# Optimization experiments

Hardware: AMD Instinct MI355X
Metric: run time of the kernel (lower is better)

The kernel has to match this reference:

```python
import jax, jax.numpy as jnp
import numpy as np
from jax import lax

WIN = 9  # box-filter window per spatial dim
PAD = WIN // 2


def _box_sum(x, filt):
    # x: [N,1,D,H,W]; uniform ones filter -> local sums, 'same' padding
    return lax.conv_general_dilated(
        x, filt, window_strides=(1, 1, 1),
        padding=[(PAD, PAD)] * 3,
        dimension_numbers=("NCDHW", "OIDHW", "NCDHW"))


def l_ncc(I, J):
    filt = jnp.ones((1, 1, WIN, WIN, WIN), dtype=I.dtype)
    win_size = float(WIN ** 3)
    I_sum = _box_sum(I, filt)
    J_sum = _box_sum(J, filt)
    I2_sum = _box_sum(I * I, filt)
    J2_sum = _box_sum(J * J, filt)
    IJ_sum = _box_sum(I * J, filt)
    u_I = I_sum / win_size
    u_J = J_sum / win_size
    cross = IJ_sum - u_J * I_sum - u_I * J_sum + u_I * u_J * win_size
    I_var = I2_sum - 2.0 * u_I * I_sum + u_I * u_I * win_size
    J_var = J2_sum - 2.0 * u_J * J_sum + u_J * u_J * win_size
    cc = cross * cross / (I_var * J_var + 1e-5)
    return 1.0 - jnp.mean(cc)


def l_mse(y_true, y_pred):
    return jnp.mean((y_true - y_pred) ** 2)


def l_smooth(s):
    # squared forward differences along the three spatial axes of [N,C,D,H,W]
    dy = s[..., 1:, :, :] - s[..., :-1, :, :]
    dx = s[..., :, 1:, :] - s[..., :, :-1, :]
    dz = s[..., :, :, 1:] - s[..., :, :, :-1]
    d = jnp.mean(dx * dx) + jnp.mean(dy * dy) + jnp.mean(dz * dz)
    return d / 3.0


def setup_inputs() -> dict:
    key = jax.random.key(0)
    k1, k2, k3, k4 = jax.random.split(key, 4)
    shp = (2, 1, 128, 128, 128)
    return {
        "imgsA": jax.random.uniform(k1, shp, dtype=jnp.float32),
        "recon_A": jax.random.uniform(k2, shp, dtype=jnp.float32),
        "warped_BA": jax.random.uniform(k3, shp, dtype=jnp.float32),
        "flow_BA": jax.random.normal(k4, (2, 3, 128, 128, 128), dtype=jnp.float32),
    }


def reference(imgsA, recon_A, warped_BA, flow_BA):
    ncc_loss = l_ncc(warped_BA, imgsA)
    mse_loss = l_mse(imgsA, recon_A)
    smooth_loss = l_smooth(flow_BA)
    return (ncc_loss, mse_loss, smooth_loss)
```

## Files before the change

### kernel.cpp

```cpp
#include <hip/hip_runtime.h>

#define VOL   4194304
#define FLOWN 12582912
#define SMCNT 12484608.0f
#define WIN_INV (1.0f / 729.0f)

__device__ __forceinline__ void block_reduce_atomic(float v, float* red, float* dst) {
#pragma unroll
    for (int off = 32; off; off >>= 1) v += __shfl_down(v, off);
    if ((threadIdx.x & 63) == 0) red[threadIdx.x >> 6] = v;
    __syncthreads();
    if (threadIdx.x == 0) atomicAdd(dst, red[0] + red[1] + red[2] + red[3]);
}

struct __align__(16) NccLds {
    float wst[2][5][16][25];
    float hst[2][5][16][16];
};

#define WSLIDE(c, X0,X1,X2,X3,X4,X5,X6,X7,X8,X9,X10,X11)                   \
    {                                                                      \
        const float o0 = X0+X1+X2+X3+X4+X5+X6+X7+X8;                       \
        const float o1 = o0 - X0 + X9;                                     \
        const float o2 = o1 - X1 + X10;                                    \
        const float o3 = o2 - X2 + X11;                                    \
        L->wst[wpl][c][wq4 + 0][wrr] = o0;                                 \
        L->wst[wpl][c][wq4 + 1][wrr] = o1;                                 \
        L->wst[wpl][c][wq4 + 2][wrr] = o2;                                 \
        L->wst[wpl][c][wq4 + 3][wrr] = o3;                                 \
    }

#define EMIT {                                                             \
        const float cross = S[4] - S[0] * S[1] * WIN_INV;                  \
        const float iv    = S[2] - S[0] * S[0] * WIN_INV;                  \
        const float jv    = S[3] - S[1] * S[1] * WIN_INV;                  \
        local += cross * cross / (iv * jv + 1e-5f);                       \
    }

#define NCC_PAIR(PP, R0, R1, R2, R3, R4, R5)                                   \
    {                                                                          \
        const int pp = (PP);                                                   \
        {                                                                      \
            const int dp = d0 - 4 + 2 * pp + wpl;                              \
            if (tid < 192 && (unsigned)dp < 128u) {                            \
                const float4 i0 = R0, i1 = R1, i2 = R2;                        \
                const float4 j0 = R3, j1 = R4, j2 = R5;                        \
                WSLIDE(0, i0.x,i0.y,i0.z,i0.w, i1.x,i1.y,i1.z,i1.w,            \
                          i2.x,i2.y,i2.z,i2.w)                                 \
                WSLIDE(1, j0.x,j0.y,j0.z,j0.w, j1.x,j1.y,j1.z,j1.w,            \
                          j2.x,j2.y,j2.z,j2.w)                                 \
                WSLIDE(2, i0.x*i0.x,i0.y*i0.y,i0.z*i0.z,i0.w*i0.w,             \
                          i1.x*i1.x,i1.y*i1.y,i1.z*i1.z,i1.w*i1.w,             \
                          i2.x*i2.x,i2.y*i2.y,i2.z*i2.z,i2.w*i2.w)             \
                WSLIDE(3, j0.x*j0.x,j0.y*j0.y,j0.z*j0.z,j0.w*j0.w,             \
                          j1.x*j1.x,j1.y*j1.y,j1.z*j1.z,j1.w*j1.w,             \
                          j2.x*j2.x,j2.y*j2.y,j2.z*j2.z,j2.w*j2.w)             \
                WSLIDE(4, i0.x*j0.x,i0.y*j0.y,i0.z*j0.z,i0.w*j0.w,             \
                          i1.x*j1.x,i1.y*j1.y,i1.z*j1.z,i1.w*j1.w,             \
                          i2.x*j2.x,i2.y*j2.y,i2.z*j2.z,i2.w*j2.w)             \
            }                                                                  \
        }                                                                      \
        if (pp + 2 < 36) issue6(pp + 2, R0, R1, R2, R3, R4, R5);               \
        __syncthreads();                                                       \
        _Pragma("unroll")                                                      \
        for (int rep = 0; rep < 3; ++rep) {                                    \
            int id = -1;                                                       \
            if (rep < 2) id = tid + rep * 256;                                 \
            else if (tid >= 128) id = 384 + tid;                               \
            if (id >= 0 && id < 640) {                                         \
                const int pl = id >= 320;                                      \
                const int r2 = id - pl * 320;                                  \
                const int c  = r2 >> 6;                                        \
                const int w  = (r2 >> 2) & 15;                                 \
                const int qh = r2 & 3;                                         \
                const int dp = d0 - 4 + 2 * pp + pl;                           \
                if ((unsigned)dp < 128u) {                                     \
                    const float* sp = &L->wst[pl][c][w][qh << 2];              \
                    const float4 a0 = *(const float4*)sp;                      \
                    const float4 a1 = *(const float4*)(sp + 4);                \
                    const float4 a2 = *(const float4*)(sp + 8);                \
                    const float o0 = a0.x+a0.y+a0.z+a0.w+a1.x+a1.y+a1.z+a1.w+a2.x; \
                    const float o1 = o0 - a0.x + a2.y;                         \
                    const float o2 = o1 - a0.y + a2.z;                         \
                    const float o3 = o2 - a0.z + a2.w;                         \
                    *(float4*)&L->hst[pl][c][w][qh << 2] =                     \
                        make_float4(o0, o1, o2, o3);                           \
                }                                                              \
            }                                                                  \
        }                                                                      \
        __syncthreads();                                                       \
        {                                                                      \
            const int dp0 = d0 - 4 + 2 * pp;                                   \
            float p0[5], p1[5];                                                \
            if ((unsigned)dp0 < 128u) {                                        \
                _Pragma("unroll")                                              \
                for (int c = 0; c < 5; ++c) p0[c] = L->hst[0][c][tw][th];      \
            } else {                                                           \
                _Pragma("unroll")                                              \
                for (int c = 0; c < 5; ++c) p0[c] = 0.f;                       \
            }                                                                  \
            if ((unsigned)(dp0 + 1) < 128u) {                                  \
                _Pragma("unroll")                                              \
                for (int c = 0; c < 5; ++c) p1[c] = L->hst[1][c][tw][th];      \
            } else {                                                           \
                _Pragma("unroll")                                              \
                for (int c = 0; c < 5; ++c) p1[c] = 0.f;                       \
            }                                                                  \
            _Pragma("unroll")                                                  \
            for (int c = 0; c < 5; ++c) S[c] += p0[c] - hist[c][8];            \
            if (pp >= 4) EMIT                                                  \
            _Pragma("unroll")                                                  \
            for (int c = 0; c < 5; ++c) S[c] += p1[c] - hist[c][7];            \
            if (pp >= 4) EMIT                                                  \
            _Pragma("unroll")                                                  \
            for (int c = 0; c < 5; ++c) {                                      \
                hist[c][8] = hist[c][6]; hist[c][7] = hist[c][5];              \
                hist[c][6] = hist[c][4]; hist[c][5] = hist[c][3];              \
                hist[c][4] = hist[c][2]; hist[c][3] = hist[c][1];              \
                hist[c][2] = hist[c][0];                                       \
                hist[c][1] = p0[c];                                            \
                hist[c][0] = p1[c];                                            \
            }                                                                  \
        }                                                                      \
    }

__device__ void ncc_block(const float* __restrict__ I, const float* __restrict__ J,
                          float* __restrict__ acc, NccLds* L, float* red, int nb) {
    const int wt = nb & 7, ht = (nb >> 3) & 7, dc = (nb >> 6) & 1, n = nb >> 7;
    const int w0 = wt << 4, h0 = ht << 4, d0 = dc << 6;
    const int tid = threadIdx.x;
    const int th = tid & 15;
    const int tw = tid >> 4;

    const int wpl = tid / 96;
    const int wit = tid - wpl * 96;
    const int wrr = wit >> 2;
    const int wq4 = (wit & 3) << 2;
    const int gh  = h0 - 4 + wrr;
    const int gwb = w0 + wq4 - 4;
    const bool wthr = (tid < 192) && ((unsigned)gh < 128u);

    float hist[5][9];
#pragma unroll
    for (int c = 0; c < 5; ++c)
#pragma unroll
        for (int k = 0; k < 9; ++k) hist[c][k] = 0.f;
    float S[5] = {0.f, 0.f, 0.f, 0.f, 0.f};
    float local = 0.f;
    const long nbase = (long)n * 2097152;

    float4 A0, A1, A2, A3, A4, A5;
    float4 B0, B1, B2, B3, B4, B5;

    auto issue6 = [&](int pp, float4& r0, float4& r1, float4& r2,
                      float4& r3, float4& r4, float4& r5) {
        const int dp = d0 - 4 + 2 * pp + wpl;
        const float4 z4 = make_float4(0.f, 0.f, 0.f, 0.f);
        r0 = r1 = r2 = r3 = r4 = r5 = z4;
        if (wthr && (unsigned)dp < 128u) {
            const float* Ip = I + nbase + (long)dp * 16384 + gh * 128 + gwb;
            const float* Jp = J + nbase + (long)dp * 16384 + gh * 128 + gwb;
            if (gwb >= 0)   { r0 = *(const float4*)Ip;       r3 = *(const float4*)Jp; }
            r1 = *(const float4*)(Ip + 4);                   r4 = *(const float4*)(Jp + 4);
            if (gwb <= 116) { r2 = *(const float4*)(Ip + 8); r5 = *(const float4*)(Jp + 8); }
        }
    };

    __builtin_amdgcn_s_setprio(1);
    issue6(0, A0, A1, A2, A3, A4, A5);
    issue6(1, B0, B1, B2, B3, B4, B5);
#pragma unroll 1
    for (int pq = 0; pq < 36; pq += 2) {
        NCC_PAIR(pq,     A0, A1, A2, A3, A4, A5)
        NCC_PAIR(pq + 1, B0, B1, B2, B3, B4, B5)
    }
    __builtin_amdgcn_s_setprio(0);
    block_reduce_atomic(local, red, &acc[0]);
}

__device__ void mse_block(const float4* __restrict__ a, const float4* __restrict__ b,
                          float* __restrict__ acc, float* red, int mb) {
    float local = 0.f;
    for (int i = mb * 256 + threadIdx.x; i < VOL / 4; i += 512 * 256) {
        const float4 x = a[i], y = b[i];
        const float d0 = x.x - y.x, d1 = x.y - y.y, d2 = x.z - y.z, d3 = x.w - y.w;
        local += d0 * d0 + d1 * d1 + d2 * d2 + d3 * d3;
    }
    block_reduce_atomic(local, red, &acc[1]);
}

__device__ void smooth_block(const float4* __restrict__ s,
                             float* __restrict__ acc, float* red, int sb) {
    float local = 0.f;
    for (int f = sb * 256 + threadIdx.x; f < FLOWN / 4; f += 2048 * 256) {
        const int w4 = f & 31, h = (f >> 5) & 127, d = (f >> 12) & 127;
        const float4 v = s[f];
        const float t1 = v.y - v.x, t2 = v.z - v.y, t3 = v.w - v.z;
        local += t1 * t1 + t2 * t2 + t3 * t3;
        if (w4 < 31) {
            const float nx = ((const float*)s)[4 * f + 4];
            const float t = nx - v.w;
            local += t * t;
        }
        if (h < 127) {
            const float4 nh = s[f + 32];
            const float u0 = nh.x - v.x, u1 = nh.y - v.y, u2 = nh.z - v.z, u3 = nh.w - v.w;
            local += u0 * u0 + u1 * u1 + u2 * u2 + u3 * u3;
        }
        if (d < 127) {
            const float4 nd = s[f + 4096];
            const float u0 = nd.x - v.x, u1 = nd.y - v.y, u2 = nd.z - v.z, u3 = nd.w - v.w;
            local += u0 * u0 + u1 * u1 + u2 * u2 + u3 * u3;
        }
    }
    block_reduce_atomic(local, red, &acc[2]);
}

__global__ __launch_bounds__(256) void fused_k(const float* __restrict__ imgsA,
                                               const float* __restrict__ recon,
                                               const float* __restrict__ warped,
                                               const float* __restrict__ flow,
                                               float* __restrict__ acc) {
    __shared__ NccLds Lsh;
    __shared__ float red[4];
    const int g = blockIdx.x;
    if (g < 256) {
        ncc_block(warped, imgsA, acc, &Lsh, red, g);
    } else {
        const int x = g - 256;
        const int q = x / 5, r = x - q * 5;
        if (r == 0) mse_block((const float4*)imgsA, (const float4*)recon, acc, red, q);
        else        smooth_block((const float4*)flow, acc, red, q * 4 + (r - 1));
    }
}

__global__ void fin_k(const float* __restrict__ acc, float* __restrict__ out) {
    if (threadIdx.x == 0) {
        out[0] = 1.0f - acc[0] * (1.0f / (float)VOL);
        out[1] = acc[1] * (1.0f / (float)VOL);
        out[2] = acc[2] * (1.0f / (3.0f * SMCNT));
    }
}

extern "C" void kernel_launch(void* const* d_in, const int* in_sizes, int n_in,
                              void* d_out, int out_size, void* d_ws, size_t ws_size,
                              hipStream_t stream) {
    const float* imgsA  = (const float*)d_in[0];
    const float* recon  = (const float*)d_in[1];
    const float* warped = (const float*)d_in[2];
    const float* flow   = (const float*)d_in[3];
    float* out = (float*)d_out;
    float* acc = (float*)d_ws;

    hipMemsetAsync(d_ws, 0, 16, stream);
    fused_k<<<2816, 256, 0, stream>>>(imgsA, recon, warped, flow, acc);
    fin_k<<<1, 64, 0, stream>>>(acc, out);
}
```

Before: 72.63 us.

## Pipeline NCC box filter per plane with one barrier and smaller depth chunks

Restructures the NCC block so each step handles one depth plane instead of a pair. W-slide, H-slide and depth accumulation for different planes are staged across consecutive steps using double-buffered LDS, which leaves a single barrier per step. The depth-history shift is replaced by a ring buffer indexed through a switch. Depth chunks drop from 64 to 32, doubling the NCC block count to 512. The extra blocks add more redundant halo planes (40 loaded per 32 output instead of 72 per 64), and only 96 threads issue global loads per plane.

```diff
diff --git a/kernel.cpp b/kernel.cpp
--- a/kernel.cpp
+++ b/kernel.cpp
@@ -13,21 +13,26 @@
     if (threadIdx.x == 0) atomicAdd(dst, red[0] + red[1] + red[2] + red[3]);
 }
 
+__device__ __forceinline__ void lds_barrier() {
+    asm volatile("s_waitcnt lgkmcnt(0)" ::: "memory");
+    __builtin_amdgcn_s_barrier();
+}
+
 struct __align__(16) NccLds {
     float wst[2][5][16][25];
     float hst[2][5][16][16];
 };
 
-#define WSLIDE(c, X0,X1,X2,X3,X4,X5,X6,X7,X8,X9,X10,X11)                   \
+#define WSLIDE(P, c, X0,X1,X2,X3,X4,X5,X6,X7,X8,X9,X10,X11)                \
     {                                                                      \
         const float o0 = X0+X1+X2+X3+X4+X5+X6+X7+X8;                       \
         const float o1 = o0 - X0 + X9;                                     \
         const float o2 = o1 - X1 + X10;                                    \
         const float o3 = o2 - X2 + X11;                                    \
-        L->wst[wpl][c][wq4 + 0][wrr] = o0;                                 \
-        L->wst[wpl][c][wq4 + 1][wrr] = o1;                                 \
-        L->wst[wpl][c][wq4 + 2][wrr] = o2;                                 \
-        L->wst[wpl][c][wq4 + 3][wrr] = o3;                                 \
+        L->wst[P][c][wq4 + 0][wrr] = o0;                                   \
+        L->wst[P][c][wq4 + 1][wrr] = o1;                                   \
+        L->wst[P][c][wq4 + 2][wrr] = o2;                                   \
+        L->wst[P][c][wq4 + 3][wrr] = o3;                                   \
     }
 
 #define EMIT {                                                             \
@@ -37,45 +42,46 @@
         local += cross * cross / (iv * jv + 1e-5f);                       \
     }
 
-#define NCC_PAIR(PP, R0, R1, R2, R3, R4, R5)                                   \
+#define RING_CASE(K)                                                       \
+    { _Pragma("unroll")                                                    \
+      for (int c = 0; c < 5; ++c) { S[c] += p[c] - hist[c][K];             \
+                                    hist[c][K] = p[c]; } }
+
+#define NCC_STEP(S_, P_)                                                       \
     {                                                                          \
-        const int pp = (PP);                                                   \
-        {                                                                      \
-            const int dp = d0 - 4 + 2 * pp + wpl;                              \
-            if (tid < 192 && (unsigned)dp < 128u) {                            \
-                const float4 i0 = R0, i1 = R1, i2 = R2;                        \
-                const float4 j0 = R3, j1 = R4, j2 = R5;                        \
-                WSLIDE(0, i0.x,i0.y,i0.z,i0.w, i1.x,i1.y,i1.z,i1.w,            \
-                          i2.x,i2.y,i2.z,i2.w)                                 \
-                WSLIDE(1, j0.x,j0.y,j0.z,j0.w, j1.x,j1.y,j1.z,j1.w,            \
-                          j2.x,j2.y,j2.z,j2.w)                                 \
-                WSLIDE(2, i0.x*i0.x,i0.y*i0.y,i0.z*i0.z,i0.w*i0.w,             \
-                          i1.x*i1.x,i1.y*i1.y,i1.z*i1.z,i1.w*i1.w,             \
-                          i2.x*i2.x,i2.y*i2.y,i2.z*i2.z,i2.w*i2.w)             \
-                WSLIDE(3, j0.x*j0.x,j0.y*j0.y,j0.z*j0.z,j0.w*j0.w,             \
-                          j1.x*j1.x,j1.y*j1.y,j1.z*j1.z,j1.w*j1.w,             \
-                          j2.x*j2.x,j2.y*j2.y,j2.z*j2.z,j2.w*j2.w)             \
-                WSLIDE(4, i0.x*j0.x,i0.y*j0.y,i0.z*j0.z,i0.w*j0.w,             \
-                          i1.x*j1.x,i1.y*j1.y,i1.z*j1.z,i1.w*j1.w,             \
-                          i2.x*j2.x,i2.y*j2.y,i2.z*j2.z,i2.w*j2.w)             \
+        const int s = (S_);                                                    \
+             \
+        if (s < 40) {                                                          \
+            const int dp = d0 - 4 + s;                                         \
+            if (wthr && (unsigned)dp < 128u) {                                 \
+                const float4 i0 = P0, i1 = P1, i2 = P2;                        \
+                const float4 j0 = P3, j1 = P4, j2 = P5;                        \
+                WSLIDE(P_, 0, i0.x,i0.y,i0.z,i0.w, i1.x,i1.y,i1.z,i1.w,        \
+                              i2.x,i2.y,i2.z,i2.w)                             \
+                WSLIDE(P_, 1, j0.x,j0.y,j0.z,j0.w, j1.x,j1.y,j1.z,j1.w,        \
+                              j2.x,j2.y,j2.z,j2.w)                             \
+                WSLIDE(P_, 2, i0.x*i0.x,i0.y*i0.y,i0.z*i0.z,i0.w*i0.w,         \
+                              i1.x*i1.x,i1.y*i1.y,i1.z*i1.z,i1.w*i1.w,         \
+                              i2.x*i2.x,i2.y*i2.y,i2.z*i2.z,i2.w*i2.w)         \
+                WSLIDE(P_, 3, j0.x*j0.x,j0.y*j0.y,j0.z*j0.z,j0.w*j0.w,         \
+                              j1.x*j1.x,j1.y*j1.y,j1.z*j1.z,j1.w*j1.w,         \
+                              j2.x*j2.x,j2.y*j2.y,j2.z*j2.z,j2.w*j2.w)         \
+                WSLIDE(P_, 4, i0.x*j0.x,i0.y*j0.y,i0.z*j0.z,i0.w*j0.w,         \
+                              i1.x*j1.x,i1.y*j1.y,i1.z*j1.z,i1.w*j1.w,         \
+                              i2.x*j2.x,i2.y*j2.y,i2.z*j2.z,i2.w*j2.w)         \
             }                                                                  \
         }                                                                      \
-        if (pp + 2 < 36) issue6(pp + 2, R0, R1, R2, R3, R4, R5);               \
-        __syncthreads();                                                       \
-        _Pragma("unroll")                                                      \
-        for (int rep = 0; rep < 3; ++rep) {                                    \
-            int id = -1;                                                       \
-            if (rep < 2) id = tid + rep * 256;                                 \
-            else if (tid >= 128) id = 384 + tid;                               \
-            if (id >= 0 && id < 640) {                                         \
-                const int pl = id >= 320;                                      \
-                const int r2 = id - pl * 320;                                  \
-                const int c  = r2 >> 6;                                        \
-                const int w  = (r2 >> 2) & 15;                                 \
-                const int qh = r2 & 3;                                         \
-                const int dp = d0 - 4 + 2 * pp + pl;                           \
-                if ((unsigned)dp < 128u) {                                     \
-                    const float* sp = &L->wst[pl][c][w][qh << 2];              \
+        if (s + 1 < 40) issue6(s + 1);               \
+             \
+        if (s >= 1 && s <= 40) {                                               \
+            _Pragma("unroll")                                                  \
+            for (int rep = 0; rep < 2; ++rep) {                                \
+                const int id = (rep == 0) ? tid : (tid >= 192 ? tid + 64 : -1);\
+                if (id >= 0) {                                                 \
+                    const int c  = id >> 6;                                    \
+                    const int w  = (id >> 2) & 15;                             \
+                    const int qh = id & 3;                                     \
+                    const float* sp = &L->wst[1 - (P_)][c][w][qh << 2];        \
                     const float4 a0 = *(const float4*)sp;                      \
                     const float4 a1 = *(const float4*)(sp + 4);                \
                     const float4 a2 = *(const float4*)(sp + 8);                \
@@ -83,62 +89,53 @@
                     const float o1 = o0 - a0.x + a2.y;                         \
                     const float o2 = o1 - a0.y + a2.z;                         \
                     const float o3 = o2 - a0.z + a2.w;                         \
-                    *(float4*)&L->hst[pl][c][w][qh << 2] =                     \
+                    *(float4*)&L->hst[1 - (P_)][c][w][qh << 2] =               \
                         make_float4(o0, o1, o2, o3);                           \
                 }                                                              \
             }                                                                  \
         }                                                                      \
-        __syncthreads();                                                       \
-        {                                                                      \
-            const int dp0 = d0 - 4 + 2 * pp;                                   \
-            float p0[5], p1[5];                                                \
-            if ((unsigned)dp0 < 128u) {                                        \
+           \
+        if (s >= 2) {                                                          \
+            const int j  = s - 2;                                              \
+            const int dpj = d0 - 4 + j;                                        \
+            float p[5];                                                        \
+            if ((unsigned)dpj < 128u) {                                        \
                 _Pragma("unroll")                                              \
-                for (int c = 0; c < 5; ++c) p0[c] = L->hst[0][c][tw][th];      \
+                for (int c = 0; c < 5; ++c) p[c] = L->hst[P_][c][tw][th];      \
             } else {                                                           \
                 _Pragma("unroll")                                              \
-                for (int c = 0; c < 5; ++c) p0[c] = 0.f;                       \
-            }                                                                  \
-            if ((unsigned)(dp0 + 1) < 128u) {                                  \
-                _Pragma("unroll")                                              \
-                for (int c = 0; c < 5; ++c) p1[c] = L->hst[1][c][tw][th];      \
-            } else {                                                           \
-                _Pragma("unroll")                                              \
-                for (int c = 0; c < 5; ++c) p1[c] = 0.f;                       \
-            }                                                                  \
-            _Pragma("unroll")                                                  \
-            for (int c = 0; c < 5; ++c) S[c] += p0[c] - hist[c][8];            \
-            if (pp >= 4) EMIT                                                  \
-            _Pragma("unroll")                                                  \
-            for (int c = 0; c < 5; ++c) S[c] += p1[c] - hist[c][7];            \
-            if (pp >= 4) EMIT                                                  \
-            _Pragma("unroll")                                                  \
-            for (int c = 0; c < 5; ++c) {                                      \
-                hist[c][8] = hist[c][6]; hist[c][7] = hist[c][5];              \
-                hist[c][6] = hist[c][4]; hist[c][5] = hist[c][3];              \
-                hist[c][4] = hist[c][2]; hist[c][3] = hist[c][1];              \
-                hist[c][2] = hist[c][0];                                       \
-                hist[c][1] = p0[c];                                            \
-                hist[c][0] = p1[c];                                            \
-            }                                                                  \
+                for (int c = 0; c < 5; ++c) p[c] = 0.f;                        \
+            }                                                                  \
+            switch (r) {                                                       \
+                case 0: RING_CASE(0) break;                                    \
+                case 1: RING_CASE(1) break;                                    \
+                case 2: RING_CASE(2) break;                                    \
+                case 3: RING_CASE(3) break;                                    \
+                case 4: RING_CASE(4) break;                                    \
+                case 5: RING_CASE(5) break;                                    \
+                case 6: RING_CASE(6) break;                                    \
+                case 7: RING_CASE(7) break;                                    \
+                default: RING_CASE(8) break;                                   \
+            }                                                                  \
+            r = (r == 8) ? 0 : r + 1;                                          \
+            if (j >= 8) EMIT                                                   \
         }                                                                      \
+        lds_barrier();                                                         \
     }
 
 __device__ void ncc_block(const float* __restrict__ I, const float* __restrict__ J,
                           float* __restrict__ acc, NccLds* L, float* red, int nb) {
-    const int wt = nb & 7, ht = (nb >> 3) & 7, dc = (nb >> 6) & 1, n = nb >> 7;
-    const int w0 = wt << 4, h0 = ht << 4, d0 = dc << 6;
+    const int wt = nb & 7, ht = (nb >> 3) & 7, dc = (nb >> 6) & 3, n = nb >> 8;
+    const int w0 = wt << 4, h0 = ht << 4, d0 = dc << 5;
     const int tid = threadIdx.x;
     const int th = tid & 15;
     const int tw = tid >> 4;
 
-    const int wpl = tid / 96;
-    const int wit = tid - wpl * 96;
-    const int wrr = wit >> 2;
-    const int wq4 = (wit & 3) << 2;
+    const int wrr = tid >> 2;
+    const int wq4 = (tid & 3) << 2;
     const int gh  = h0 - 4 + wrr;
     const int gwb = w0 + wq4 - 4;
-    const bool wthr = (tid < 192) && ((unsigned)gh < 128u);
+    const bool wthr = (tid < 96) && ((unsigned)gh < 128u);
 
     float hist[5][9];
 #pragma unroll
@@ -147,32 +144,30 @@
         for (int k = 0; k < 9; ++k) hist[c][k] = 0.f;
     float S[5] = {0.f, 0.f, 0.f, 0.f, 0.f};
     float local = 0.f;
+    int r = 0;
     const long nbase = (long)n * 2097152;
 
-    float4 A0, A1, A2, A3, A4, A5;
-    float4 B0, B1, B2, B3, B4, B5;
-
-    auto issue6 = [&](int pp, float4& r0, float4& r1, float4& r2,
-                      float4& r3, float4& r4, float4& r5) {
-        const int dp = d0 - 4 + 2 * pp + wpl;
+    float4 P0, P1, P2, P3, P4, P5;
+
+    auto issue6 = [&](int s) {
+        const int dp = d0 - 4 + s;
         const float4 z4 = make_float4(0.f, 0.f, 0.f, 0.f);
-        r0 = r1 = r2 = r3 = r4 = r5 = z4;
+        P0 = P1 = P2 = P3 = P4 = P5 = z4;
         if (wthr && (unsigned)dp < 128u) {
             const float* Ip = I + nbase + (long)dp * 16384 + gh * 128 + gwb;
             const float* Jp = J + nbase + (long)dp * 16384 + gh * 128 + gwb;
-            if (gwb >= 0)   { r0 = *(const float4*)Ip;       r3 = *(const float4*)Jp; }
-            r1 = *(const float4*)(Ip + 4);                   r4 = *(const float4*)(Jp + 4);
-            if (gwb <= 116) { r2 = *(const float4*)(Ip + 8); r5 = *(const float4*)(Jp + 8); }
+            if (gwb >= 0)   { P0 = *(const float4*)Ip;       P3 = *(const float4*)Jp; }
+            P1 = *(const float4*)(Ip + 4);                   P4 = *(const float4*)(Jp + 4);
+            if (gwb <= 116) { P2 = *(const float4*)(Ip + 8); P5 = *(const float4*)(Jp + 8); }
         }
     };
 
     __builtin_amdgcn_s_setprio(1);
-    issue6(0, A0, A1, A2, A3, A4, A5);
-    issue6(1, B0, B1, B2, B3, B4, B5);
+    issue6(0);
 #pragma unroll 1
-    for (int pq = 0; pq < 36; pq += 2) {
-        NCC_PAIR(pq,     A0, A1, A2, A3, A4, A5)
-        NCC_PAIR(pq + 1, B0, B1, B2, B3, B4, B5)
+    for (int ss = 0; ss <= 40; ss += 2) {
+        NCC_STEP(ss, 0)
+        NCC_STEP(ss + 1, 1)
     }
     __builtin_amdgcn_s_setprio(0);
     block_reduce_atomic(local, red, &acc[0]);
@@ -224,10 +219,10 @@
     __shared__ NccLds Lsh;
     __shared__ float red[4];
     const int g = blockIdx.x;
-    if (g < 256) {
+    if (g < 512) {
         ncc_block(warped, imgsA, acc, &Lsh, red, g);
     } else {
-        const int x = g - 256;
+        const int x = g - 512;
         const int q = x / 5, r = x - q * 5;
         if (r == 0) mse_block((const float4*)imgsA, (const float4*)recon, acc, red, q);
         else        smooth_block((const float4*)flow, acc, red, q * 4 + (r - 1));
@@ -253,6 +248,6 @@
     float* acc = (float*)d_ws;
 
     hipMemsetAsync(d_ws, 0, 16, stream);
-    fused_k<<<2816, 256, 0, stream>>>(imgsA, recon, warped, flow, acc);
+    fused_k<<<3072, 256, 0, stream>>>(imgsA, recon, warped, flow, acc);
     fin_k<<<1, 64, 0, stream>>>(acc, out);
 }
```

Measured after the change: 84.24 us. +16.0%, slower.
